# Kernel optimization log

Hardware: AMD Instinct MI355X
Metric: run time of the kernel (lower is better)

Reference implementation:

```python
import jax, jax.numpy as jnp
import numpy as np

N = 50000
E = 600000
IN1, IN2, HID, OUT = 256, 128, 128, 64


def gcn_conv(x, W, b, src, dst, n):
    """PyG GCNConv: D^{-1/2}(A+I)D^{-1/2} X W + b with self-loops."""
    h = x @ W  # [N, F_out]
    # degree including self-loop (edge weight 1)
    deg = jax.ops.segment_sum(jnp.ones_like(dst, dtype=h.dtype), dst, num_segments=n) + 1.0
    dinv = deg ** -0.5
    coef = dinv[src] * dinv[dst]  # [E]
    agg = jax.ops.segment_sum(h[src] * coef[:, None], dst, num_segments=n)
    agg = agg + h * (dinv * dinv)[:, None]  # self-loop contribution
    return agg + b


def gcn_stack(x, edge_index, Ws, bs, n):
    src, dst = edge_index[0], edge_index[1]
    x = jax.nn.relu(gcn_conv(x, Ws[0], bs[0], src, dst, n))
    return gcn_conv(x, Ws[1], bs[1], src, dst, n)


def setup_inputs() -> dict:
    key = jax.random.key(0)
    ks = jax.random.split(key, 12)
    glorot = lambda k, fi, fo: jax.random.normal(k, (fi, fo), jnp.float32) * np.sqrt(2.0 / (fi + fo))
    return {
        "x1": jax.random.normal(ks[0], (N, IN1), jnp.float32),
        "edge_index1": jax.random.randint(ks[1], (2, E), 0, N, jnp.int32),
        "x2": jax.random.normal(ks[2], (N, IN2), jnp.float32),
        "edge_index2": jax.random.randint(ks[3], (2, E), 0, N, jnp.int32),
        "W1_0": glorot(ks[4], IN1, HID), "b1_0": jnp.zeros((HID,), jnp.float32),
        "W1_1": glorot(ks[5], HID, OUT), "b1_1": jnp.zeros((OUT,), jnp.float32),
        "W2_0": glorot(ks[6], IN2, HID), "b2_0": jnp.zeros((HID,), jnp.float32),
        "W2_1": glorot(ks[7], HID, OUT), "b2_1": jnp.zeros((OUT,), jnp.float32),
    }


def reference(x1, edge_index1, x2, edge_index2,
              W1_0, b1_0, W1_1, b1_1, W2_0, b2_0, W2_1, b2_1):
    out1 = gcn_stack(x1, edge_index1, (W1_0, W1_1), (b1_0, b1_1), N)
    out2 = gcn_stack(x2, edge_index2, (W2_0, W2_1), (b2_0, b2_1), N)
    return out1, out2
```

## Files before the change

kernel.cpp:

```cpp
#include <hip/hip_runtime.h>
#include <hip/hip_bf16.h>
#include <cstdint>
#include <type_traits>

static constexpr int NN = 50000;
static constexpr int NE = 600000;
static constexpr int NB = (NN + 255) / 256;
static constexpr int CHUNK = 1024;
static constexpr int NCH = (NE + CHUNK - 1) / CHUNK;
static constexpr int CAP = 4096;

typedef __bf16 bf16;
typedef __attribute__((ext_vector_type(2))) __bf16 bf16x2;
typedef __attribute__((ext_vector_type(8))) __bf16 bf16x8;
typedef __attribute__((ext_vector_type(4))) float f32x4;

__global__ __launch_bounds__(256) void k_wprep4(const float* __restrict__ WA,
                                                const float* __restrict__ WB,
                                                const float* __restrict__ WC,
                                                const float* __restrict__ WD,
                                                bf16* __restrict__ wf0,
                                                bf16* __restrict__ wf1,
                                                int* __restrict__ bucketcur,
                                                int* __restrict__ row_off) {
    int y = blockIdx.y;
    int i = blockIdx.x * 256 + threadIdx.x;
    if (y == 4) {
        if (i < 2 * NB) bucketcur[i] = i * CAP;
        if (i < 2) row_off[i * (NN + 1) + NN] = NE;
        return;
    }
    const float* W = (y == 0) ? WA : (y == 1) ? WB : (y == 2) ? WC : WD;
    bf16* wf = (y == 0) ? wf0 : (y == 1) ? wf0 + 256 * 128 : (y == 2) ? wf1 : wf1 + 128 * 64;
    int K = (y == 0) ? 256 : 128;
    int F = (y <= 1) ? 128 : 64;
    if (i < K * F) {
        int k = i / F, n = i % F;
        wf[((size_t)(k >> 3) * F + n) * 8 + (k & 7)] = (bf16)W[i];
    }
}

template <int K, int F, typename AT>
__device__ __forceinline__ void gemm_body(const AT* __restrict__ X,
                                          const bf16* __restrict__ wf,
                                          bf16* __restrict__ H, int n, int bx) {
    constexpr int NT = F / 16;
    int wave = threadIdx.x >> 6;
    int lane = threadIdx.x & 63;
    int lm = lane & 15;
    int lk = lane >> 4;
    int r0 = bx * 64 + wave * 16;

    int arow = r0 + lm;
    if (arow >= n) arow = n - 1;
    const AT* xrow = X + (size_t)arow * K;

    f32x4 acc[NT] = {};

    for (int k0 = 0; k0 < K; k0 += 32) {
        bf16x8 af;
        if constexpr (std::is_same_v<AT, float>) {
            f32x4 a0 = *reinterpret_cast<const f32x4*>(xrow + k0 + lk * 8);
            f32x4 a1 = *reinterpret_cast<const f32x4*>(xrow + k0 + lk * 8 + 4);
            af[0] = (bf16)a0.x; af[1] = (bf16)a0.y; af[2] = (bf16)a0.z; af[3] = (bf16)a0.w;
            af[4] = (bf16)a1.x; af[5] = (bf16)a1.y; af[6] = (bf16)a1.z; af[7] = (bf16)a1.w;
        } else {
            af = *reinterpret_cast<const bf16x8*>(xrow + k0 + lk * 8);
        }
        const bf16* wbase = wf + ((size_t)(k0 / 8 + lk) * F) * 8;
        #pragma unroll
        for (int t = 0; t < NT; ++t) {
            bf16x8 bfg = *reinterpret_cast<const bf16x8*>(wbase + (t * 16 + lm) * 8);
            acc[t] = __builtin_amdgcn_mfma_f32_16x16x32_bf16(af, bfg, acc[t], 0, 0, 0);
        }
    }

    #pragma unroll
    for (int t = 0; t < NT; ++t) {
        #pragma unroll
        for (int i = 0; i < 4; ++i) {
            int gr = r0 + lk * 4 + i;
            if (gr < n) H[(size_t)gr * F + t * 16 + lm] = (bf16)acc[t][i];
        }
    }
}

static constexpr int GB = (NN + 63) / 64;

__global__ __launch_bounds__(256) void k_mega(const float* __restrict__ x1,
                                              const float* __restrict__ x2,
                                              const bf16* __restrict__ wf0,
                                              bf16* __restrict__ h,
                                              const int* __restrict__ srcA,
                                              const int* __restrict__ dstA,
                                              const int* __restrict__ srcB,
                                              const int* __restrict__ dstB,
                                              int* __restrict__ bucketcur,
                                              int2* __restrict__ stg) {
    __shared__ int cnt[NB];
    __shared__ int ibase[NB];
    int bx = blockIdx.x;
    if (bx < 2 * GB) {
        if (bx < GB)
            gemm_body<256, 128, float>(x1, wf0, h, NN, bx);
        else
            gemm_body<128, 128, float>(x2, wf0 + 256 * 128, h + (size_t)NN * 128, NN, bx - GB);
        return;
    }
    int cx = bx - 2 * GB;
    int g = (cx >= NCH);
    int chunk = cx - g * NCH;
    const int* src = g ? srcB : srcA;
    const int* dst = g ? dstB : dstA;
    int tid = threadIdx.x;
    int c0 = chunk * CHUNK;
    if (tid < NB) cnt[tid] = 0;
    __syncthreads();
    #pragma unroll
    for (int it = 0; it < CHUNK / 256; ++it) {
        int e = c0 + it * 256 + tid;
        if (e < NE) atomicAdd(&cnt[dst[e] >> 8], 1);
    }
    __syncthreads();
    if (tid < NB) {
        int c = cnt[tid];
        ibase[tid] = c ? atomicAdd(&bucketcur[g * NB + tid], c) : 0;
        cnt[tid] = 0;
    }
    __syncthreads();
    #pragma unroll
    for (int it = 0; it < CHUNK / 256; ++it) {
        int e = c0 + it * 256 + tid;
        if (e < NE) {
            int s = src[e], d = dst[e];
            int b = d >> 8;
            int p = atomicAdd(&cnt[b], 1);
            stg[(size_t)ibase[b] + p] = make_int2(s, d);
        }
    }
}

__global__ __launch_bounds__(256) void k_binB1(const int2* __restrict__ stg,
                                               const int* __restrict__ bucketcur,
                                               int* __restrict__ row_off,
                                               float* __restrict__ dinv) {
    __shared__ int cnt[256];
    __shared__ int s[256];
    __shared__ int bb[256];
    int g = blockIdx.y;
    int b = blockIdx.x;
    int B = g * NB + b;
    int tid = threadIdx.x;

    int cv = (tid < NB) ? bucketcur[g * NB + tid] - (g * NB + tid) * CAP : 0;
    s[tid] = cv;
    __syncthreads();
    for (int off = 1; off < 256; off <<= 1) {
        int t = (tid >= off) ? s[tid - off] : 0;
        __syncthreads();
        s[tid] += t;
        __syncthreads();
    }
    if (tid < NB) bb[tid] = s[tid] - cv;
    cnt[tid] = 0;
    __syncthreads();
    int base = bb[b];

    int node0 = b << 8;
    int nnod = min(256, NN - node0);
    int count = bucketcur[B] - B * CAP;
    const int2* s0 = stg + (size_t)B * CAP;
    for (int j = tid; j < count; j += 256)
        atomicAdd(&cnt[s0[j].y - node0], 1);
    __syncthreads();
    int v = cnt[tid];
    s[tid] = v;
    __syncthreads();
    for (int off = 1; off < 256; off <<= 1) {
        int t = (tid >= off) ? s[tid - off] : 0;
        __syncthreads();
        s[tid] += t;
        __syncthreads();
    }
    if (tid < nnod) {
        row_off[g * (NN + 1) + node0 + tid] = base + s[tid] - v;
        dinv[(size_t)g * NN + node0 + tid] = rsqrtf((float)v + 1.0f);
    }
}

__global__ __launch_bounds__(256) void k_binB2(const int2* __restrict__ stg,
                                               const int* __restrict__ bucketcur,
                                               const int* __restrict__ row_off,
                                               const float* __restrict__ dinv,
                                               int2* __restrict__ pair) {
    __shared__ int lcur[256];
    __shared__ float ldv[256];
    int g = blockIdx.y;
    int b = blockIdx.x;
    int B = g * NB + b;
    int tid = threadIdx.x;
    int node0 = b << 8;
    int nnod = min(256, NN - node0);
    const int* ro = row_off + g * (NN + 1);
    if (tid < nnod) {
        lcur[tid] = ro[node0 + tid];
        ldv[tid] = dinv[(size_t)g * NN + node0 + tid];
    }
    __syncthreads();
    int count = bucketcur[B] - B * CAP;
    const int2* s0 = stg + (size_t)B * CAP;
    for (int j = tid; j < count; j += 256) {
        int2 sd = s0[j];
        int rel = sd.y - node0;
        int pos = atomicAdd(&lcur[rel], 1);
        float cf = dinv[(size_t)g * NN + sd.x] * ldv[rel];
        pair[(size_t)g * NE + pos] = make_int2(sd.x, __float_as_int(cf));
    }
}

__global__ __launch_bounds__(256) void gemm_l2(const bf16* __restrict__ a,
                                               const bf16* __restrict__ wf1,
                                               bf16* __restrict__ h2) {
    int bx = blockIdx.x;
    int g = (bx >= GB);
    gemm_body<128, 64, bf16>(a + (size_t)g * NN * 128, wf1 + g * 128 * 64,
                             h2 + (size_t)g * NN * 64, NN, bx - g * GB);
}

__global__ __launch_bounds__(256) void agg128_2(const bf16* __restrict__ hb,
                                                const int* __restrict__ row_off,
                                                const int2* __restrict__ pairb,
                                                const float* __restrict__ dinv,
                                                const float* __restrict__ biasA,
                                                const float* __restrict__ biasB,
                                                bf16* __restrict__ ab) {
    int wid = blockIdx.x * 4 + (threadIdx.x >> 6);
    if (wid >= 2 * NN) return;
    int g = (wid >= NN);
    int node = wid - g * NN;
    int lane = threadIdx.x & 63;

    const bf16* h = hb + (size_t)g * NN * 128;
    const int2* pair = pairb + (size_t)g * NE;
    const int* ro = row_off + g * (NN + 1);
    const float* bias = g ? biasB : biasA;

    int f = lane * 2;
    float di = dinv[g * NN + node];
    int beg = ro[node];
    int end = ro[node + 1];

    float a0 = 0.f, a1 = 0.f;

    auto edge1 = [&](int2 p) {
        float c = __int_as_float(p.y);
        bf16x2 v = *reinterpret_cast<const bf16x2*>(&h[(size_t)p.x * 128 + f]);
        a0 = fmaf((float)v[0], c, a0); a1 = fmaf((float)v[1], c, a1);
    };
    auto edge2 = [&](int4 q) {
        float cA = __int_as_float(q.y), cB = __int_as_float(q.w);
        bf16x2 vA = *reinterpret_cast<const bf16x2*>(&h[(size_t)q.x * 128 + f]);
        bf16x2 vB = *reinterpret_cast<const bf16x2*>(&h[(size_t)q.z * 128 + f]);
        a0 = fmaf((float)vA[0], cA, a0); a1 = fmaf((float)vA[1], cA, a1);
        a0 = fmaf((float)vB[0], cB, a0); a1 = fmaf((float)vB[1], cB, a1);
    };

    int j = beg;
    if ((j & 1) && j < end) { edge1(pair[j]); ++j; }
    for (; j + 7 < end; j += 8) {
        int4 q0 = *reinterpret_cast<const int4*>(&pair[j]);
        int4 q1 = *reinterpret_cast<const int4*>(&pair[j + 2]);
        int4 q2 = *reinterpret_cast<const int4*>(&pair[j + 4]);
        int4 q3 = *reinterpret_cast<const int4*>(&pair[j + 6]);
        edge2(q0); edge2(q1); edge2(q2); edge2(q3);
    }
    for (; j + 1 < end; j += 2) {
        int4 q = *reinterpret_cast<const int4*>(&pair[j]);
        edge2(q);
    }
    if (j < end) edge1(pair[j]);

    bf16x2 hv = *reinterpret_cast<const bf16x2*>(&h[(size_t)node * 128 + f]);
    float sc = di * di;
    a0 = fmaf((float)hv[0], sc, a0) + bias[f];
    a1 = fmaf((float)hv[1], sc, a1) + bias[f + 1];
    a0 = fmaxf(a0, 0.f);
    a1 = fmaxf(a1, 0.f);

    bf16x2 r;
    r[0] = (bf16)a0; r[1] = (bf16)a1;
    *reinterpret_cast<bf16x2*>(&ab[((size_t)g * NN + node) * 128 + f]) = r;
}

__global__ __launch_bounds__(256) void agg64_2(const bf16* __restrict__ h2b,
                                               const int* __restrict__ row_off,
                                               const int2* __restrict__ pairb,
                                               const float* __restrict__ dinv,
                                               const float* __restrict__ biasA,
                                               const float* __restrict__ biasB,
                                               float* __restrict__ outb) {
    int wid = blockIdx.x * 4 + (threadIdx.x >> 6);
    if (wid >= 2 * NN) return;
    int g = (wid >= NN);
    int node = wid - g * NN;
    int lane = threadIdx.x & 63;

    const bf16* h = h2b + (size_t)g * NN * 64;
    const int2* pair = pairb + (size_t)g * NE;
    const int* ro = row_off + g * (NN + 1);
    const float* bias = g ? biasB : biasA;
    float* out = outb + (size_t)g * NN * 64;

    int half = lane >> 5;
    int f = (lane & 31) * 2;
    float di = dinv[(size_t)g * NN + node];
    int beg = ro[node];
    int end = ro[node + 1];

    float a0 = 0.f, a1 = 0.f;

    auto edge = [&](int2 p) {
        float c = __int_as_float(p.y);
        bf16x2 v = *reinterpret_cast<const bf16x2*>(&h[(size_t)p.x * 64 + f]);
        a0 = fmaf((float)v[0], c, a0); a1 = fmaf((float)v[1], c, a1);
    };

    int j = beg;
    for (; j + 7 < end; j += 8) {
        int2 p0 = pair[j + half], p1 = pair[j + 2 + half];
        int2 p2 = pair[j + 4 + half], p3 = pair[j + 6 + half];
        edge(p0); edge(p1); edge(p2); edge(p3);
    }
    for (; j + 1 < end; j += 2) edge(pair[j + half]);
    if (j < end && half == 0) edge(pair[j]);

    a0 += __shfl_xor(a0, 32);
    a1 += __shfl_xor(a1, 32);

    bf16x2 hv = *reinterpret_cast<const bf16x2*>(&h[(size_t)node * 64 + f]);
    float sc = di * di;
    a0 = fmaf((float)hv[0], sc, a0) + bias[f];
    a1 = fmaf((float)hv[1], sc, a1) + bias[f + 1];

    if (half == 0) {
        out[(size_t)node * 64 + f] = a0;
        out[(size_t)node * 64 + f + 1] = a1;
    }
}

extern "C" void kernel_launch(void* const* d_in, const int* in_sizes, int n_in,
                              void* d_out, int out_size, void* d_ws, size_t ws_size,
                              hipStream_t stream) {
    const float* x1 = (const float*)d_in[0];
    const int* ei1 = (const int*)d_in[1];
    const float* x2 = (const float*)d_in[2];
    const int* ei2 = (const int*)d_in[3];
    const float* W1_0 = (const float*)d_in[4];
    const float* b1_0 = (const float*)d_in[5];
    const float* W1_1 = (const float*)d_in[6];
    const float* b1_1 = (const float*)d_in[7];
    const float* W2_0 = (const float*)d_in[8];
    const float* b2_0 = (const float*)d_in[9];
    const float* W2_1 = (const float*)d_in[10];
    const float* b2_1 = (const float*)d_in[11];

    float* out = (float*)d_out;

    char* ws = (char*)d_ws;
    size_t off = 0;
    auto alloc = [&](size_t bytes) {
        size_t o = off;
        off = (off + bytes + 255) & ~(size_t)255;
        return o;
    };
    bf16* h = (bf16*)(ws + alloc((size_t)2 * NN * 128 * 2));
    size_t r2 = (size_t)2 * NB * CAP * 8;
    char* region2 = ws + alloc(r2);
    int2* stg = (int2*)region2;
    bf16* h2 = (bf16*)region2;
    bf16* a = (bf16*)(ws + alloc((size_t)2 * NN * 128 * 2));
    int2* pair = (int2*)(ws + alloc((size_t)2 * NE * 8));
    int* row_off = (int*)(ws + alloc((size_t)2 * (NN + 1) * 4));
    float* dinv = (float*)(ws + alloc((size_t)2 * NN * 4));
    int* bucketcur = (int*)(ws + alloc((size_t)2 * NB * 4));
    bf16* wf0 = (bf16*)(ws + alloc((size_t)2 * 256 * 128 * 2));
    bf16* wf1 = (bf16*)(ws + alloc((size_t)2 * 128 * 64 * 2));

    const int* srcA = ei1, *dstA = ei1 + NE;
    const int* srcB = ei2, *dstB = ei2 + NE;

    k_wprep4<<<dim3(128, 5), 256, 0, stream>>>(W1_0, W2_0, W1_1, W2_1, wf0, wf1,
                                               bucketcur, row_off);
    k_mega<<<2 * GB + 2 * NCH, 256, 0, stream>>>(x1, x2, wf0, h,
                                                 srcA, dstA, srcB, dstB, bucketcur, stg);
    k_binB1<<<dim3(NB, 2), 256, 0, stream>>>(stg, bucketcur, row_off, dinv);
    k_binB2<<<dim3(NB, 2), 256, 0, stream>>>(stg, bucketcur, row_off, dinv, pair);

    agg128_2<<<(2 * NN + 3) / 4, 256, 0, stream>>>(h, row_off, pair, dinv, b1_0, b2_0, a);
    gemm_l2<<<2 * GB, 256, 0, stream>>>(a, wf1, h2);
    agg64_2<<<(2 * NN + 3) / 4, 256, 0, stream>>>(h2, row_off, pair, dinv, b1_1, b2_1, out);
}
```

Baseline: 193.0 us.

## Sort edge chunks in LDS before scatter, pre-scale pair indices, reorder blocks

The edge-binning blocks now stage each chunk in shared memory, do a block-wide prefix scan over bucket counts, and then write the staging buffer in bucket-contiguous order, so global scatter writes become more coalesced. Binning blocks are also moved ahead of the GEMM blocks in the grid so they get scheduled first. The pair array now stores the source index pre-shifted into a byte offset, which removes the 64-bit multiply in the aggregation gathers. The cost is extra shared memory and syncs in the binning path, and the shifted index assumes it fits in 32 bits.

```diff
diff --git a/kernel.cpp b/kernel.cpp
--- a/kernel.cpp
+++ b/kernel.cpp
@@ -97,23 +97,27 @@
                                               const int* __restrict__ dstB,
                                               int* __restrict__ bucketcur,
                                               int2* __restrict__ stg) {
+    __shared__ int2 sorted[CHUNK];
     __shared__ int cnt[NB];
+    __shared__ int lbase[NB];
     __shared__ int ibase[NB];
     int bx = blockIdx.x;
-    if (bx < 2 * GB) {
-        if (bx < GB)
-            gemm_body<256, 128, float>(x1, wf0, h, NN, bx);
+    if (bx >= 2 * NCH) {
+        int gx = bx - 2 * NCH;
+        if (gx < GB)
+            gemm_body<256, 128, float>(x1, wf0, h, NN, gx);
         else
-            gemm_body<128, 128, float>(x2, wf0 + 256 * 128, h + (size_t)NN * 128, NN, bx - GB);
+            gemm_body<128, 128, float>(x2, wf0 + 256 * 128, h + (size_t)NN * 128, NN, gx - GB);
         return;
     }
-    int cx = bx - 2 * GB;
-    int g = (cx >= NCH);
-    int chunk = cx - g * NCH;
+    int g = (bx >= NCH);
+    int chunk = bx - g * NCH;
     const int* src = g ? srcB : srcA;
     const int* dst = g ? dstB : dstA;
     int tid = threadIdx.x;
     int c0 = chunk * CHUNK;
+    int total = min(CHUNK, NE - c0);
+
     if (tid < NB) cnt[tid] = 0;
     __syncthreads();
     #pragma unroll
@@ -122,9 +126,21 @@
         if (e < NE) atomicAdd(&cnt[dst[e] >> 8], 1);
     }
     __syncthreads();
+    int* s = reinterpret_cast<int*>(sorted);
+    int v = (tid < NB) ? cnt[tid] : 0;
+    s[tid] = v;
+    __syncthreads();
+    for (int off = 1; off < 256; off <<= 1) {
+        int t = (tid >= off) ? s[tid - off] : 0;
+        __syncthreads();
+        s[tid] += t;
+        __syncthreads();
+    }
+    int incl = s[tid];
+    __syncthreads();
     if (tid < NB) {
-        int c = cnt[tid];
-        ibase[tid] = c ? atomicAdd(&bucketcur[g * NB + tid], c) : 0;
+        lbase[tid] = incl - v;
+        ibase[tid] = v ? atomicAdd(&bucketcur[g * NB + tid], v) : 0;
         cnt[tid] = 0;
     }
     __syncthreads();
@@ -132,11 +148,17 @@
     for (int it = 0; it < CHUNK / 256; ++it) {
         int e = c0 + it * 256 + tid;
         if (e < NE) {
-            int s = src[e], d = dst[e];
+            int sv = src[e], d = dst[e];
             int b = d >> 8;
             int p = atomicAdd(&cnt[b], 1);
-            stg[(size_t)ibase[b] + p] = make_int2(s, d);
+            sorted[lbase[b] + p] = make_int2(sv, d);
         }
+    }
+    __syncthreads();
+    for (int p = tid; p < total; p += 256) {
+        int2 sd = sorted[p];
+        int b = sd.y >> 8;
+        stg[(size_t)ibase[b] + (p - lbase[b])] = sd;
     }
 }
 
@@ -214,7 +236,7 @@
         int rel = sd.y - node0;
         int pos = atomicAdd(&lcur[rel], 1);
         float cf = dinv[(size_t)g * NN + sd.x] * ldv[rel];
-        pair[(size_t)g * NE + pos] = make_int2(sd.x, __float_as_int(cf));
+        pair[(size_t)g * NE + pos] = make_int2(sd.x << 8, __float_as_int(cf));
     }
 }
 
@@ -241,11 +263,13 @@
     int lane = threadIdx.x & 63;
 
     const bf16* h = hb + (size_t)g * NN * 128;
+    const char* hB = reinterpret_cast<const char*>(h);
     const int2* pair = pairb + (size_t)g * NE;
     const int* ro = row_off + g * (NN + 1);
     const float* bias = g ? biasB : biasA;
 
     int f = lane * 2;
+    int fb = lane * 4;
     float di = dinv[g * NN + node];
     int beg = ro[node];
     int end = ro[node + 1];
@@ -254,13 +278,13 @@
 
     auto edge1 = [&](int2 p) {
         float c = __int_as_float(p.y);
-        bf16x2 v = *reinterpret_cast<const bf16x2*>(&h[(size_t)p.x * 128 + f]);
+        bf16x2 v = *reinterpret_cast<const bf16x2*>(hB + (unsigned)p.x + fb);
         a0 = fmaf((float)v[0], c, a0); a1 = fmaf((float)v[1], c, a1);
     };
     auto edge2 = [&](int4 q) {
         float cA = __int_as_float(q.y), cB = __int_as_float(q.w);
-        bf16x2 vA = *reinterpret_cast<const bf16x2*>(&h[(size_t)q.x * 128 + f]);
-        bf16x2 vB = *reinterpret_cast<const bf16x2*>(&h[(size_t)q.z * 128 + f]);
+        bf16x2 vA = *reinterpret_cast<const bf16x2*>(hB + (unsigned)q.x + fb);
+        bf16x2 vB = *reinterpret_cast<const bf16x2*>(hB + (unsigned)q.z + fb);
         a0 = fmaf((float)vA[0], cA, a0); a1 = fmaf((float)vA[1], cA, a1);
         a0 = fmaf((float)vB[0], cB, a0); a1 = fmaf((float)vB[1], cB, a1);
     };
@@ -306,6 +330,7 @@
     int lane = threadIdx.x & 63;
 
     const bf16* h = h2b + (size_t)g * NN * 64;
+    const char* hB = reinterpret_cast<const char*>(h);
     const int2* pair = pairb + (size_t)g * NE;
     const int* ro = row_off + g * (NN + 1);
     const float* bias = g ? biasB : biasA;
@@ -313,6 +338,7 @@
 
     int half = lane >> 5;
     int f = (lane & 31) * 2;
+    int fb = (lane & 31) * 4;
     float di = dinv[(size_t)g * NN + node];
     int beg = ro[node];
     int end = ro[node + 1];
@@ -321,7 +347,7 @@
 
     auto edge = [&](int2 p) {
         float c = __int_as_float(p.y);
-        bf16x2 v = *reinterpret_cast<const bf16x2*>(&h[(size_t)p.x * 64 + f]);
+        bf16x2 v = *reinterpret_cast<const bf16x2*>(hB + (((unsigned)p.x) >> 1) + fb);
         a0 = fmaf((float)v[0], c, a0); a1 = fmaf((float)v[1], c, a1);
     };
 
@@ -391,7 +417,7 @@
 
     k_wprep4<<<dim3(128, 5), 256, 0, stream>>>(W1_0, W2_0, W1_1, W2_1, wf0, wf1,
                                                bucketcur, row_off);
-    k_mega<<<2 * GB + 2 * NCH, 256, 0, stream>>>(x1, x2, wf0, h,
+    k_mega<<<2 * NCH + 2 * GB, 256, 0, stream>>>(x1, x2, wf0, h,
                                                  srcA, dstA, srcB, dstB, bucketcur, stg);
     k_binB1<<<dim3(NB, 2), 256, 0, stream>>>(stg, bucketcur, row_off, dinv);
     k_binB2<<<dim3(NB, 2), 256, 0, stream>>>(stg, bucketcur, row_off, dinv, pair);
```

After: 188.4 us. 2.4% less time.
